# Kernel tuning notes

Hardware: AMD Instinct MI355X
Metric: run time of the kernel (lower is better)

## Reference

```python
import jax, jax.numpy as jnp
import numpy as np

# ---- box encoding helpers ----

def _cv2_corners(b):
    # b: [..., 5] (cx, cy, w, h, angle) -> [..., 4, 2] rotated-rect vertices
    cx, cy, w, h, a = (b[..., i] for i in range(5))
    c, s = jnp.cos(a), jnp.sin(a)
    dx, dy = w * 0.5, h * 0.5
    lx = jnp.stack([-dx, dx, dx, -dx], axis=-1)   # [..., 4]
    ly = jnp.stack([-dy, -dy, dy, dy], axis=-1)
    x = cx[..., None] + lx * c[..., None] - ly * s[..., None]
    y = cy[..., None] + lx * s[..., None] + ly * c[..., None]
    return jnp.stack([x, y], axis=-1)


def _vertices_to_cv2(v):
    # v: [..., 4, 2] ordered vertices -> [..., 5] (cx, cy, w, h, angle)
    ctr = v.mean(axis=-2)
    e1 = v[..., 1, :] - v[..., 0, :]
    e2 = v[..., 3, :] - v[..., 0, :]
    w = jnp.linalg.norm(e1, axis=-1)
    h = jnp.linalg.norm(e2, axis=-1)
    ang = jnp.arctan2(e1[..., 1], e1[..., 0])
    return jnp.concatenate([ctr, w[..., None], h[..., None], ang[..., None]], axis=-1)


def _corners_to_hbb(corners):
    # [..., 4, 2] -> [..., 4] (x1, y1, x2, y2)
    return jnp.concatenate([corners.min(axis=-2), corners.max(axis=-2)], axis=-1)


def _box_iou(a, b):
    # a: [B, N, 4], b: [B, M, 4] -> [B, N, M] axis-aligned IoU
    lt = jnp.maximum(a[:, :, None, :2], b[:, None, :, :2])
    rb = jnp.minimum(a[:, :, None, 2:], b[:, None, :, 2:])
    wh = jnp.clip(rb - lt, 0.0)
    inter = wh[..., 0] * wh[..., 1]
    area_a = (a[..., 2] - a[..., 0]) * (a[..., 3] - a[..., 1])
    area_b = (b[..., 2] - b[..., 0]) * (b[..., 3] - b[..., 1])
    union = area_a[:, :, None] + area_b[:, None, :] - inter
    return inter / jnp.clip(union, 1e-7)


def setup_inputs() -> dict:
    key = jax.random.key(0)
    ks = jax.random.split(key, 6)
    B, N, M, C = 8, 16384, 128, 81

    def rand_boxes(k, shape):
        k1, k2, k3 = jax.random.split(k, 3)
        ctr = jax.random.uniform(k1, shape + (2,), minval=0.0, maxval=1000.0)
        wh = jax.random.uniform(k2, shape + (2,), minval=16.0, maxval=160.0)
        ang = jax.random.uniform(k3, shape + (1,), minval=-1.5, maxval=1.5)
        return jnp.concatenate([ctr, wh, ang], axis=-1)

    box_pred = rand_boxes(ks[0], (B, N))
    gt = rand_boxes(ks[1], (B, M))
    # seed the first M predictions near the GT so positives (IoU>=0.5) exist
    box_pred = box_pred.at[:, :M].set(gt + 2.0 * jax.random.normal(ks[2], gt.shape))
    regression_targets = _cv2_corners(gt)                     # [B, M, 4, 2] vertices
    classification_targets = jax.random.randint(ks[3], (B, M), 0, C - 1)
    class_pred = jax.random.normal(ks[4], (B, N, C))
    return {
        "box_pred": box_pred,
        "class_pred": class_pred,
        "regression_targets": regression_targets,
        "classification_targets": classification_targets,
        "n_samples": 256,
    }


def reference(box_pred, class_pred, regression_targets, classification_targets, n_samples):
    B = box_pred.shape[0]
    C = class_pred.shape[-1]
    background_cls = C - 1
    k_pos = n_samples // 2
    k_neg = n_samples - k_pos

    box_targets_cv2 = _vertices_to_cv2(regression_targets)           # [B, M, 5]
    hbb_pred = _corners_to_hbb(_cv2_corners(box_pred))               # [B, N, 4]
    hbb_tgt = _corners_to_hbb(regression_targets)                    # [B, M, 4]
    iou = _box_iou(hbb_pred, hbb_tgt)                                # [B, N, M]

    def per_image(iou_i, labels_i, logits_i, boxp_i, boxt_i):
        max_iou = iou_i.max(axis=-1)                                 # [N]
        match = iou_i.argmax(axis=-1)                                # [N] matched GT idx
        pos_mask = max_iou >= 0.5
        # sample up to k_pos positives (highest IoU) and k_neg negatives (lowest IoU)
        pos_score = jnp.where(pos_mask, max_iou, -1.0)
        _, pos_idx = jax.lax.top_k(pos_score, k_pos)
        pos_valid = pos_mask[pos_idx]
        neg_score = jnp.where(pos_mask, -jnp.inf, -max_iou)
        _, neg_idx = jax.lax.top_k(neg_score, k_neg)
        neg_valid = ~pos_mask[neg_idx]
        # classification targets: matched GT label for positives, background otherwise
        cls_target = jnp.where(pos_mask, labels_i[match], background_cls)
        sel_idx = jnp.concatenate([pos_idx, neg_idx])                # [n_samples]
        sel_valid = jnp.concatenate([pos_valid, neg_valid])
        logp = jax.nn.log_softmax(logits_i[sel_idx], axis=-1)        # [n_samples, C]
        nll = -jnp.take_along_axis(logp, cls_target[sel_idx][:, None], axis=1)[:, 0]
        cls_loss = jnp.sum(nll * sel_valid.astype(logp.dtype))
        rel_pred = boxp_i[pos_idx]                                   # [k_pos, 5]
        rel_gt = boxt_i[match[pos_idx]]                              # [k_pos, 5]
        d = jnp.abs(rel_pred - rel_gt)
        sl1 = jnp.where(d < 1.0, 0.5 * d * d, d - 0.5)
        regr_loss = jnp.sum(sl1 * pos_valid[:, None].astype(sl1.dtype))
        return cls_loss, regr_loss

    cls_l, reg_l = jax.vmap(per_image)(
        iou, classification_targets, class_pred, box_pred, box_targets_cv2
    )
    classification_loss = cls_l.sum() / B
    regression_loss = reg_l.sum() / B
    total_loss = classification_loss + regression_loss
    return total_loss, classification_loss, regression_loss
```

## Files before the change

kernel.cpp:

```cpp
#include <hip/hip_runtime.h>
#include <math.h>

#define B_ 8
#define N_ 16384
#define M_ 128
#define C_ 81
#define TPB 512
#define KPT 32
#define NWAVE (TPB / 64)

__global__ __launch_bounds__(256)
void iou_fused(const float* __restrict__ bp,
               const float* __restrict__ rt,
               float* __restrict__ miou,
               int* __restrict__ match,
               float* __restrict__ out) {
    __shared__ float sx1[M_], sy1[M_], sx2[M_], sy2[M_], sab[M_];
    int b = blockIdx.y;
    int n = blockIdx.x * blockDim.x + threadIdx.x;

    if (blockIdx.x == 0 && blockIdx.y == 0 && threadIdx.x < 3)
        out[threadIdx.x] = 0.0f;

    if (threadIdx.x < M_) {
        const float* v = rt + ((size_t)b * M_ + threadIdx.x) * 8;
        float x0 = v[0], y0 = v[1], x1 = v[2], y1 = v[3];
        float x2 = v[4], y2 = v[5], x3 = v[6], y3 = v[7];
        float mnx = fminf(fminf(x0, x1), fminf(x2, x3));
        float mny = fminf(fminf(y0, y1), fminf(y2, y3));
        float mxx = fmaxf(fmaxf(x0, x1), fmaxf(x2, x3));
        float mxy = fmaxf(fmaxf(y0, y1), fmaxf(y2, y3));
        sx1[threadIdx.x] = mnx; sy1[threadIdx.x] = mny;
        sx2[threadIdx.x] = mxx; sy2[threadIdx.x] = mxy;
        sab[threadIdx.x] = (mxx - mnx) * (mxy - mny);
    }
    __syncthreads();

    const float* p = bp + ((size_t)b * N_ + n) * 5;
    float cx = p[0], cy = p[1], w = p[2], h = p[3], a = p[4];
    float c = cosf(a), s = sinf(a);
    float dx = w * 0.5f, dy = h * 0.5f;
    float ex = fabsf(dx * c) + fabsf(dy * s);
    float ey = fabsf(dx * s) + fabsf(dy * c);
    float ax1 = cx - ex, ay1 = cy - ey, ax2 = cx + ex, ay2 = cy + ey;
    float area_a = (ax2 - ax1) * (ay2 - ay1);

    float bin = -1.0f, bun = 1.0f;
    int bm = 0;
#pragma unroll 4
    for (int m = 0; m < M_; m++) {
        float lx = fmaxf(ax1, sx1[m]), ly = fmaxf(ay1, sy1[m]);
        float rx = fminf(ax2, sx2[m]), ry = fminf(ay2, sy2[m]);
        float ww = fmaxf(rx - lx, 0.0f), hh = fmaxf(ry - ly, 0.0f);
        float inter = ww * hh;
        float uni = fmaxf(area_a + sab[m] - inter, 1e-7f);
        bool better = inter * bun > bin * uni;
        bin = better ? inter : bin;
        bun = better ? uni : bun;
        bm = better ? m : bm;
    }
    miou[(size_t)b * N_ + n] = bin / bun;
    match[(size_t)b * N_ + n] = bm;
}

__device__ __forceinline__ unsigned wave_sum6(unsigned c) {
    unsigned s = 0;
#pragma unroll
    for (int bit = 0; bit < 6; bit++)
        s += (unsigned)__popcll(__ballot((c >> bit) & 1u)) << bit;
    return s;
}

__device__ __forceinline__ unsigned bsum(unsigned c, unsigned* slot) {
    unsigned ws = wave_sum6(c);
    if ((threadIdx.x & 63) == 0) slot[threadIdx.x >> 6] = ws;
    __syncthreads();
    unsigned r = 0;
#pragma unroll
    for (int i = 0; i < NWAVE; i++) r += slot[i];
    return r;
}

__global__ __launch_bounds__(TPB)
void select_loss(const float* __restrict__ miou, const int* __restrict__ match,
                 const float* __restrict__ logits, const float* __restrict__ bp,
                 const float* __restrict__ rt, const int* __restrict__ labels,
                 const int* __restrict__ ns_ptr, float* __restrict__ out) {
    int type = blockIdx.x;
    int b = blockIdx.y;
    __shared__ float s_cv2[5][M_];
    __shared__ unsigned red[2 * NWAVE] __attribute__((aligned(16)));
    __shared__ float fredc[NWAVE], fredr[NWAVE];
    __shared__ unsigned sel[256];
    __shared__ unsigned selcnt;

    int tid = threadIdx.x;
    int lane = tid & 63, wv = tid >> 6;
    if (tid == 0) selcnt = 0;

    if (tid < M_) {
        const float* v = rt + ((size_t)b * M_ + tid) * 8;
        float x0 = v[0], y0 = v[1], x1 = v[2], y1 = v[3];
        float x2 = v[4], y2 = v[5], x3 = v[6], y3 = v[7];
        s_cv2[0][tid] = (x0 + x1 + x2 + x3) * 0.25f;
        s_cv2[1][tid] = (y0 + y1 + y2 + y3) * 0.25f;
        float e1x = x1 - x0, e1y = y1 - y0;
        float e2x = x3 - x0, e2y = y3 - y0;
        s_cv2[2][tid] = sqrtf(e1x * e1x + e1y * e1y);
        s_cv2[3][tid] = sqrtf(e2x * e2x + e2y * e2y);
        s_cv2[4][tid] = atan2f(e1y, e1x);
    }

    int ns = ns_ptr[0];
    unsigned ktar = (type == 0) ? (unsigned)(ns / 2) : (unsigned)(ns - ns / 2);
    if (ktar > 256u) ktar = 256u;

    const float4* mi4 = (const float4*)(miou + (size_t)b * N_);
    int base = tid * KPT;
    unsigned key[KPT];
    unsigned vcnt = 0;
#pragma unroll
    for (int q = 0; q < KPT / 4; q++) {
        float4 v4 = mi4[tid * (KPT / 4) + q];
        float io[4] = {v4.x, v4.y, v4.z, v4.w};
#pragma unroll
        for (int j = 0; j < 4; j++) {
            bool pos = (io[j] >= 0.5f);
            unsigned k;
            if (type == 0) {
                if (pos) { k = ~(__float_as_uint(io[j]) | 0x80000000u); vcnt++; }
                else k = 0xFFFFFFFFu;
            } else {
                if (!pos) { k = __float_as_uint(io[j]) | 0x80000000u; vcnt++; }
                else k = 0xFFFFFFFFu;
            }
            key[q * 4 + j] = k;
        }
    }
    __syncthreads();

    int pc = 0;
    unsigned V = bsum(vcnt, red + NWAVE * ((pc++) & 1));
    unsigned keff = (ktar < V) ? ktar : V;

    if (keff == V) {
#pragma unroll
        for (int j = 0; j < KPT; j++) {
            if (key[j] != 0xFFFFFFFFu) {
                unsigned p = atomicAdd(&selcnt, 1u);
                sel[p] = (unsigned)(base + j);
            }
        }
    } else {
        unsigned Ckey;
        bool found = false;
        if (type == 1) {
            unsigned cmin = 0;
#pragma unroll
            for (int j = 0; j < KPT; j++) cmin += (key[j] <= 0x80000000u) ? 1u : 0u;
            unsigned tot = bsum(cmin, red + NWAVE * ((pc++) & 1));
            if (tot >= keff) { Ckey = 0x80000000u; found = true; }
        }
        if (!found) {
            unsigned lo = 0, hi = 0xFFFFFFFFu;
            while (lo < hi) {
                unsigned mid = lo + ((hi - lo) >> 1);
                unsigned c = 0;
#pragma unroll
                for (int j = 0; j < KPT; j++) c += (key[j] <= mid) ? 1u : 0u;
                unsigned tot = bsum(c, red + NWAVE * ((pc++) & 1));
                if (tot >= keff) hi = mid; else lo = mid + 1;
            }
            Ckey = lo;
        }

        unsigned cl = 0, ce = 0;
#pragma unroll
        for (int j = 0; j < KPT; j++) {
            cl += (key[j] < Ckey) ? 1u : 0u;
            ce += (key[j] == Ckey) ? 1u : 0u;
        }
        unsigned m = bsum(cl, red + NWAVE * ((pc++) & 1));
        unsigned e = keff - m;

        unsigned sc = ce;
#pragma unroll
        for (int o = 1; o < 64; o <<= 1) {
            unsigned t = __shfl_up(sc, o);
            if (lane >= o) sc += t;
        }
        unsigned* slot = red + NWAVE * ((pc++) & 1);
        if (lane == 63) slot[wv] = sc;
        __syncthreads();
        unsigned off = 0;
        for (int i = 0; i < wv; i++) off += slot[i];
        unsigned rank = off + sc - ce;

#pragma unroll
        for (int j = 0; j < KPT; j++) {
            unsigned k = key[j];
            bool s = false;
            if (k < Ckey) s = true;
            else if (k == Ckey) { s = (rank < e); rank++; }
            if (s) {
                unsigned p = atomicAdd(&selcnt, 1u);
                sel[p] = (unsigned)(base + j);
            }
        }
    }
    __syncthreads();
    unsigned total_sel = selcnt;

    float cls_sum = 0.f, reg_sum = 0.f;
    int q = tid & 3;
    for (unsigned sm = (unsigned)(tid >> 2); sm < total_sel; sm += TPB / 4) {
        unsigned i = sel[sm];
        const float* row = logits + ((size_t)b * N_ + i) * C_;
        int c0 = q * 21;
        int c1 = (c0 + 21 < C_) ? c0 + 21 : C_;
        float mx = -INFINITY;
        for (int c = c0; c < c1; c++) mx = fmaxf(mx, row[c]);
        mx = fmaxf(mx, __shfl_xor(mx, 1));
        mx = fmaxf(mx, __shfl_xor(mx, 2));
        float se = 0.f;
        for (int c = c0; c < c1; c++) se += expf(row[c] - mx);
        se += __shfl_xor(se, 1);
        se += __shfl_xor(se, 2);
        if (q == 0) {
            float lse = mx + logf(se);
            if (type == 0) {
                int g_gt = match[(size_t)b * N_ + i];
                int tc = labels[b * M_ + g_gt];
                cls_sum += lse - row[tc];
                const float* pp = bp + ((size_t)b * N_ + i) * 5;
#pragma unroll
                for (int d = 0; d < 5; d++) {
                    float ad = fabsf(pp[d] - s_cv2[d][g_gt]);
                    reg_sum += (ad < 1.f) ? 0.5f * ad * ad : ad - 0.5f;
                }
            } else {
                cls_sum += lse - row[C_ - 1];
            }
        }
    }

#pragma unroll
    for (int o = 32; o; o >>= 1) {
        cls_sum += __shfl_down(cls_sum, o);
        reg_sum += __shfl_down(reg_sum, o);
    }
    if (lane == 0) { fredc[wv] = cls_sum; fredr[wv] = reg_sum; }
    __syncthreads();
    if (tid == 0) {
        float cs = 0.f, rs = 0.f;
#pragma unroll
        for (int i = 0; i < NWAVE; i++) { cs += fredc[i]; rs += fredr[i]; }
        const float invB = 1.0f / (float)B_;
        atomicAdd(&out[0], (cs + rs) * invB);
        atomicAdd(&out[1], cs * invB);
        atomicAdd(&out[2], rs * invB);
    }
}

extern "C" void kernel_launch(void* const* d_in, const int* in_sizes, int n_in,
                              void* d_out, int out_size, void* d_ws, size_t ws_size,
                              hipStream_t stream) {
    const float* box_pred = (const float*)d_in[0];
    const float* class_pred = (const float*)d_in[1];
    const float* reg_tgt = (const float*)d_in[2];
    const int* cls_tgt = (const int*)d_in[3];
    const int* n_samples = (const int*)d_in[4];

    float* ws = (float*)d_ws;
    float* miou = ws;
    int* match = (int*)(miou + (size_t)B_ * N_);
    float* out = (float*)d_out;

    iou_fused<<<dim3(N_ / 256, B_), 256, 0, stream>>>(box_pred, reg_tgt, miou, match, out);
    select_loss<<<dim3(2, B_), TPB, 0, stream>>>(miou, match, class_pred, box_pred,
                                                 reg_tgt, cls_tgt, n_samples, out);
}
```

Baseline: 128.3 us.

## Precompute selection keys and counts in IoU kernel, narrow binary search range

The IoU kernel now writes pre-encoded positive/negative sort keys, a byte match index, and per-block counts of positives and zero-IoU entries. The select kernel reads these keys directly, gets the valid count from the per-block counts instead of a block reduction, and starts its threshold binary search from a bounded key range, which cuts the number of reduction rounds. The aim is to shorten the serial selection phase that runs on only 16 blocks. In exchange it writes two key arrays instead of one, relies on IoU values staying in [0.5, 1] and [0, 2) for the narrowed search bounds, drops the union clamp, and packs the counts into 16-bit fields.

```diff
diff --git a/kernel.cpp b/kernel.cpp
--- a/kernel.cpp
+++ b/kernel.cpp
@@ -8,16 +8,21 @@
 #define TPB 512
 #define KPT 32
 #define NWAVE (TPB / 64)
-
-__global__ __launch_bounds__(256)
+#define ABLK 32
+#define ATPB 512
+
+__global__ __launch_bounds__(ATPB)
 void iou_fused(const float* __restrict__ bp,
                const float* __restrict__ rt,
-               float* __restrict__ miou,
-               int* __restrict__ match,
+               unsigned* __restrict__ poskey,
+               unsigned* __restrict__ negkey,
+               unsigned char* __restrict__ match8,
+               unsigned* __restrict__ cnt,
                float* __restrict__ out) {
     __shared__ float sx1[M_], sy1[M_], sx2[M_], sy2[M_], sab[M_];
+    __shared__ unsigned scnt[ATPB / 64];
     int b = blockIdx.y;
-    int n = blockIdx.x * blockDim.x + threadIdx.x;
+    int n = blockIdx.x * ATPB + threadIdx.x;
 
     if (blockIdx.x == 0 && blockIdx.y == 0 && threadIdx.x < 3)
         out[threadIdx.x] = 0.0f;
@@ -53,14 +58,31 @@
         float rx = fminf(ax2, sx2[m]), ry = fminf(ay2, sy2[m]);
         float ww = fmaxf(rx - lx, 0.0f), hh = fmaxf(ry - ly, 0.0f);
         float inter = ww * hh;
-        float uni = fmaxf(area_a + sab[m] - inter, 1e-7f);
+        float uni = area_a + sab[m] - inter;
         bool better = inter * bun > bin * uni;
         bin = better ? inter : bin;
         bun = better ? uni : bun;
         bm = better ? m : bm;
     }
-    miou[(size_t)b * N_ + n] = bin / bun;
-    match[(size_t)b * N_ + n] = bm;
+    float iou = bin / bun;
+    unsigned bits = __float_as_uint(iou);
+    bool pos = (iou >= 0.5f);
+    size_t gi = (size_t)b * N_ + n;
+    poskey[gi] = pos ? ~(bits | 0x80000000u) : 0xFFFFFFFFu;
+    negkey[gi] = pos ? 0xFFFFFFFFu : (bits | 0x80000000u);
+    match8[gi] = (unsigned char)bm;
+
+    unsigned posb = (unsigned)__popcll(__ballot(pos));
+    unsigned zerb = (unsigned)__popcll(__ballot(bits == 0u));
+    int lane = threadIdx.x & 63, wv = threadIdx.x >> 6;
+    if (lane == 0) scnt[wv] = posb | (zerb << 16);
+    __syncthreads();
+    if (threadIdx.x == 0) {
+        unsigned t = 0;
+#pragma unroll
+        for (int i = 0; i < ATPB / 64; i++) t += scnt[i];
+        cnt[(size_t)b * ABLK + blockIdx.x] = t;
+    }
 }
 
 __device__ __forceinline__ unsigned wave_sum6(unsigned c) {
@@ -82,10 +104,13 @@
 }
 
 __global__ __launch_bounds__(TPB)
-void select_loss(const float* __restrict__ miou, const int* __restrict__ match,
+void select_loss(const unsigned* __restrict__ keys_pos,
+                 const unsigned* __restrict__ keys_neg,
+                 const unsigned char* __restrict__ match8,
                  const float* __restrict__ logits, const float* __restrict__ bp,
                  const float* __restrict__ rt, const int* __restrict__ labels,
-                 const int* __restrict__ ns_ptr, float* __restrict__ out) {
+                 const int* __restrict__ ns_ptr, const unsigned* __restrict__ cnt,
+                 float* __restrict__ out) {
     int type = blockIdx.x;
     int b = blockIdx.y;
     __shared__ float s_cv2[5][M_];
@@ -93,12 +118,19 @@
     __shared__ float fredc[NWAVE], fredr[NWAVE];
     __shared__ unsigned sel[256];
     __shared__ unsigned selcnt;
+    __shared__ unsigned s_tot;
 
     int tid = threadIdx.x;
     int lane = tid & 63, wv = tid >> 6;
     if (tid == 0) selcnt = 0;
 
-    if (tid < M_) {
+    const unsigned* kb = (type == 0) ? keys_pos : keys_neg;
+    const uint4* k4 = (const uint4*)(kb + (size_t)b * N_);
+    uint4 kv[KPT / 4];
+#pragma unroll
+    for (int q = 0; q < KPT / 4; q++) kv[q] = k4[tid * (KPT / 4) + q];
+
+    if (type == 0 && tid < M_) {
         const float* v = rt + ((size_t)b * M_ + tid) * 8;
         float x0 = v[0], y0 = v[1], x1 = v[2], y1 = v[3];
         float x2 = v[4], y2 = v[5], x3 = v[6], y3 = v[7];
@@ -111,38 +143,34 @@
         s_cv2[4][tid] = atan2f(e1y, e1x);
     }
 
+    if (wv == 0) {
+        unsigned c = (lane < ABLK) ? cnt[(size_t)b * ABLK + lane] : 0u;
+#pragma unroll
+        for (int o = 1; o < 64; o <<= 1) c += __shfl_xor(c, o);
+        if (lane == 0) s_tot = c;
+    }
+
     int ns = ns_ptr[0];
     unsigned ktar = (type == 0) ? (unsigned)(ns / 2) : (unsigned)(ns - ns / 2);
     if (ktar > 256u) ktar = 256u;
 
-    const float4* mi4 = (const float4*)(miou + (size_t)b * N_);
+    unsigned key[KPT];
+#pragma unroll
+    for (int q = 0; q < KPT / 4; q++) {
+        key[q * 4 + 0] = kv[q].x; key[q * 4 + 1] = kv[q].y;
+        key[q * 4 + 2] = kv[q].z; key[q * 4 + 3] = kv[q].w;
+    }
     int base = tid * KPT;
-    unsigned key[KPT];
-    unsigned vcnt = 0;
-#pragma unroll
-    for (int q = 0; q < KPT / 4; q++) {
-        float4 v4 = mi4[tid * (KPT / 4) + q];
-        float io[4] = {v4.x, v4.y, v4.z, v4.w};
-#pragma unroll
-        for (int j = 0; j < 4; j++) {
-            bool pos = (io[j] >= 0.5f);
-            unsigned k;
-            if (type == 0) {
-                if (pos) { k = ~(__float_as_uint(io[j]) | 0x80000000u); vcnt++; }
-                else k = 0xFFFFFFFFu;
-            } else {
-                if (!pos) { k = __float_as_uint(io[j]) | 0x80000000u; vcnt++; }
-                else k = 0xFFFFFFFFu;
-            }
-            key[q * 4 + j] = k;
-        }
-    }
-    __syncthreads();
+
+    __syncthreads();
+
+    unsigned tot = s_tot;
+    unsigned pos_total = tot & 0xFFFFu;
+    unsigned zero_total = tot >> 16;
+    unsigned V = (type == 0) ? pos_total : (unsigned)N_ - pos_total;
+    unsigned keff = (ktar < V) ? ktar : V;
 
     int pc = 0;
-    unsigned V = bsum(vcnt, red + NWAVE * ((pc++) & 1));
-    unsigned keff = (ktar < V) ? ktar : V;
-
     if (keff == V) {
 #pragma unroll
         for (int j = 0; j < KPT; j++) {
@@ -152,36 +180,33 @@
             }
         }
     } else {
-        unsigned Ckey;
-        bool found = false;
-        if (type == 1) {
-            unsigned cmin = 0;
-#pragma unroll
-            for (int j = 0; j < KPT; j++) cmin += (key[j] <= 0x80000000u) ? 1u : 0u;
-            unsigned tot = bsum(cmin, red + NWAVE * ((pc++) & 1));
-            if (tot >= keff) { Ckey = 0x80000000u; found = true; }
-        }
-        if (!found) {
-            unsigned lo = 0, hi = 0xFFFFFFFFu;
+        unsigned Ckey, m;
+        bool zshort = (type == 1) && (zero_total >= keff);
+        if (zshort) {
+            Ckey = 0x80000000u;
+            m = 0u;
+        } else {
+            unsigned lo = (type == 0) ? 0x40000000u : 0x80000000u;
+            unsigned hi = (type == 0) ? 0x41000000u : 0xC0000000u;
             while (lo < hi) {
                 unsigned mid = lo + ((hi - lo) >> 1);
                 unsigned c = 0;
 #pragma unroll
                 for (int j = 0; j < KPT; j++) c += (key[j] <= mid) ? 1u : 0u;
-                unsigned tot = bsum(c, red + NWAVE * ((pc++) & 1));
-                if (tot >= keff) hi = mid; else lo = mid + 1;
+                unsigned t2 = bsum(c, red + NWAVE * ((pc++) & 1));
+                if (t2 >= keff) hi = mid; else lo = mid + 1;
             }
             Ckey = lo;
-        }
-
-        unsigned cl = 0, ce = 0;
-#pragma unroll
-        for (int j = 0; j < KPT; j++) {
-            cl += (key[j] < Ckey) ? 1u : 0u;
-            ce += (key[j] == Ckey) ? 1u : 0u;
-        }
-        unsigned m = bsum(cl, red + NWAVE * ((pc++) & 1));
+            unsigned cl = 0;
+#pragma unroll
+            for (int j = 0; j < KPT; j++) cl += (key[j] < Ckey) ? 1u : 0u;
+            m = bsum(cl, red + NWAVE * ((pc++) & 1));
+        }
         unsigned e = keff - m;
+
+        unsigned ce = 0;
+#pragma unroll
+        for (int j = 0; j < KPT; j++) ce += (key[j] == Ckey) ? 1u : 0u;
 
         unsigned sc = ce;
 #pragma unroll
@@ -229,7 +254,7 @@
         if (q == 0) {
             float lse = mx + logf(se);
             if (type == 0) {
-                int g_gt = match[(size_t)b * N_ + i];
+                int g_gt = (int)match8[(size_t)b * N_ + i];
                 int tc = labels[b * M_ + g_gt];
                 cls_sum += lse - row[tc];
                 const float* pp = bp + ((size_t)b * N_ + i) * 5;
@@ -271,12 +296,15 @@
     const int* cls_tgt = (const int*)d_in[3];
     const int* n_samples = (const int*)d_in[4];
 
-    float* ws = (float*)d_ws;
-    float* miou = ws;
-    int* match = (int*)(miou + (size_t)B_ * N_);
+    unsigned* poskey = (unsigned*)d_ws;
+    unsigned* negkey = poskey + (size_t)B_ * N_;
+    unsigned* cnt = negkey + (size_t)B_ * N_;
+    unsigned char* match8 = (unsigned char*)(cnt + B_ * ABLK);
     float* out = (float*)d_out;
 
-    iou_fused<<<dim3(N_ / 256, B_), 256, 0, stream>>>(box_pred, reg_tgt, miou, match, out);
-    select_loss<<<dim3(2, B_), TPB, 0, stream>>>(miou, match, class_pred, box_pred,
-                                                 reg_tgt, cls_tgt, n_samples, out);
-}
+    iou_fused<<<dim3(ABLK, B_), ATPB, 0, stream>>>(box_pred, reg_tgt, poskey,
+                                                   negkey, match8, cnt, out);
+    select_loss<<<dim3(2, B_), TPB, 0, stream>>>(poskey, negkey, match8,
+                                                 class_pred, box_pred, reg_tgt,
+                                                 cls_tgt, n_samples, cnt, out);
+}
```

Measured after the change: 125.8 us. 2.0% less time.
